# Optimization experiments

Hardware: AMD Instinct MI355X
Metric: run time of the kernel (lower is better)

## Reference

```python
import jax, jax.numpy as jnp
import numpy as np

B, L, CIN, COUT, HEADS = 8, 2048, 256, 256, 4
HD = COUT // HEADS
NEG_SLOPE = 0.2


def setup_inputs() -> dict:
    key = jax.random.key(0)
    k1, k2, k3, k4, k5 = jax.random.split(key, 5)
    x = jax.random.normal(k1, (B, L, CIN), dtype=jnp.float32)
    adj_mask = jax.random.randint(k2, (B, L, L), 0, 2) > 0  # bool [B,L,L]
    W = jax.random.normal(k3, (COUT, CIN), dtype=jnp.float32) * (1.0 / np.sqrt(CIN))
    att_src = jax.random.normal(k4, (1, HEADS, 1, HD), dtype=jnp.float32) * 0.1
    att_dst = jax.random.normal(k5, (1, HEADS, 1, HD), dtype=jnp.float32) * 0.1
    return {"x": x, "adj_mask": adj_mask, "W": W, "att_src": att_src, "att_dst": att_dst}


def reference(x, adj_mask, W, att_src, att_dst):
    Bb, Ll, _ = x.shape
    # linear projection (no bias), split heads: [B, H, L, D]
    h = jnp.einsum('blc,oc->blo', x, W).reshape(Bb, Ll, HEADS, HD).transpose(0, 2, 1, 3)
    # additive GAT scores
    a_src = jnp.sum(h * att_src, axis=-1, keepdims=True)          # [B,H,L,1]
    a_dst = jnp.sum(h * att_dst, axis=-1, keepdims=True)          # [B,H,L,1]
    e = a_src + jnp.swapaxes(a_dst, 2, 3)                          # [B,H,L,L]
    e = jnp.where(e >= 0, e, NEG_SLOPE * e)                        # leaky relu
    fill = jnp.finfo(e.dtype).min
    e = jnp.where(adj_mask[:, None, :, :], e, fill)                # mask non-edges
    alpha = jax.nn.softmax(e, axis=-1)                             # [B,H,L,L]
    # dropout is identity in eval/reference mode
    out = jnp.einsum('bhij,bhjd->bhid', alpha, h)                  # [B,H,L,D]
    return out.transpose(0, 2, 1, 3).reshape(Bb, Ll, COUT)
```

## Files before the change

### kernel.cpp

```cpp
#include <hip/hip_runtime.h>

#define B_ 8
#define L_ 2048
#define CIN_ 256
#define COUT_ 256
#define HEADS_ 4
#define HD_ 64
#define NEG_SLOPE_ 0.2f
#define LOG2E_ 1.4426950408889634f

#define TI 32
#define TJ 64
#define NJT (L_ / TJ)

typedef __attribute__((ext_vector_type(4))) float f32x4;
typedef __attribute__((ext_vector_type(8))) __bf16 bf16x8;
typedef __attribute__((ext_vector_type(4))) __bf16 bf16x4;


__global__ __launch_bounds__(256, 4)
void pack_kernel(const int* __restrict__ adj, unsigned long long* __restrict__ abitsT) {
  const size_t wid = ((size_t)blockIdx.x * 256 + threadIdx.x) >> 6;
  const int lane = threadIdx.x & 63;
  const int* p = adj + wid * 256 + lane;
  unsigned long long b0 = __ballot(p[0]   != 0);
  unsigned long long b1 = __ballot(p[64]  != 0);
  unsigned long long b2 = __ballot(p[128] != 0);
  unsigned long long b3 = __ballot(p[192] != 0);
  if (lane == 0) {
    const size_t row = wid >> 3;
    const int jw0 = (int)(wid & 7) * 4;
    const size_t bb = row >> 11, l = row & 2047;
    unsigned long long* dst = abitsT + (bb << 16) + l;
    dst[(size_t)(jw0 + 0) << 11] = b0;
    dst[(size_t)(jw0 + 1) << 11] = b1;
    dst[(size_t)(jw0 + 2) << 11] = b2;
    dst[(size_t)(jw0 + 3) << 11] = b3;
  }
}

__global__ __launch_bounds__(512, 2)
void proj_kernel(const float* __restrict__ x, const float* __restrict__ W,
                 const float* __restrict__ att_src, const float* __restrict__ att_dst,
                 __bf16* __restrict__ hF, float2* __restrict__ aE,
                 float2* __restrict__ aF) {
  __shared__ __align__(16) __bf16 Wl[COUT_][72];
  __shared__ __align__(16) __bf16 Al[2][2][512];

  const int tid = threadIdx.x;
  const int r0 = blockIdx.x * TI;
  const int b  = r0 >> 11;
  const int l0 = r0 & (L_ - 1);

  const int w8 = tid >> 6, lane = tid & 63, col = lane & 15, q = lane >> 4;
  const int h  = w8 & 3;
  const int mh = w8 >> 2;
  const int wrow = tid >> 3;
  const int wc8  = (tid & 7) * 8;
  const int si = tid >> 3, soct = tid & 7;

  f32x4 acc[4];
#pragma unroll
  for (int nt = 0; nt < 4; ++nt) acc[nt] = (f32x4)0.f;

  for (int kc = 0; kc < CIN_ / 64; ++kc) {
    __syncthreads();
#pragma unroll
    for (int rg = 0; rg < 4; ++rg) {
      const int row = rg * 64 + wrow;
      const float4* ws = (const float4*)(W + (size_t)row * CIN_ + kc * 64 + wc8);
#pragma unroll
      for (int u = 0; u < 2; ++u) {
        float4 f = ws[u];
        bf16x4 v;
        v[0] = (__bf16)f.x; v[1] = (__bf16)f.y; v[2] = (__bf16)f.z; v[3] = (__bf16)f.w;
        *(bf16x4*)&Wl[row][wc8 + u * 4] = v;
      }
    }
    if (tid < 256) {
      const float4* xs = (const float4*)(x + (size_t)(r0 + si) * CIN_ + kc * 64 + soct * 8);
      float4 f0 = xs[0], f1 = xs[1];
      bf16x8 v;
      v[0] = (__bf16)f0.x; v[1] = (__bf16)f0.y; v[2] = (__bf16)f0.z; v[3] = (__bf16)f0.w;
      v[4] = (__bf16)f1.x; v[5] = (__bf16)f1.y; v[6] = (__bf16)f1.z; v[7] = (__bf16)f1.w;
      *(bf16x8*)&Al[si >> 4][soct >> 2][(((soct & 3) << 4) + (si & 15)) << 3] = v;
    }
    __syncthreads();

    bf16x8 af[2], bfr[2][4];
#pragma unroll
    for (int kt = 0; kt < 2; ++kt)
      af[kt] = *(const bf16x8*)&Al[mh][kt][lane << 3];
#pragma unroll
    for (int kt = 0; kt < 2; ++kt)
#pragma unroll
      for (int nt = 0; nt < 4; ++nt)
        bfr[kt][nt] = *(const bf16x8*)&Wl[h * 64 + nt * 16 + col][kt * 32 + q * 8];
#pragma unroll
    for (int kt = 0; kt < 2; ++kt)
#pragma unroll
      for (int nt = 0; nt < 4; ++nt)
        acc[nt] = __builtin_amdgcn_mfma_f32_16x16x32_bf16(
            af[kt], bfr[kt][nt], acc[nt], 0, 0, 0);
  }

  float asv[4], adv[4];
#pragma unroll
  for (int nt = 0; nt < 4; ++nt) {
    asv[nt] = att_src[h * 64 + nt * 16 + col];
    adv[nt] = att_dst[h * 64 + nt * 16 + col];
  }
#pragma unroll
  for (int reg = 0; reg < 4; ++reg) {
    float s = 0.f, d = 0.f;
#pragma unroll
    for (int nt = 0; nt < 4; ++nt) {
      s = fmaf(acc[nt][reg], asv[nt], s);
      d = fmaf(acc[nt][reg], adv[nt], d);
    }
    s += __shfl_xor(s, 1, 64); d += __shfl_xor(d, 1, 64);
    s += __shfl_xor(s, 2, 64); d += __shfl_xor(d, 2, 64);
    s += __shfl_xor(s, 4, 64); d += __shfl_xor(d, 4, 64);
    s += __shfl_xor(s, 8, 64); d += __shfl_xor(d, 8, 64);
    if (col == 0) {
      const int il = mh * 16 + q * 4 + reg;
      const size_t idx = ((size_t)(b * HEADS_ + h) << 11) + l0 + il;
      float2 ev, fv;
      ev.x = __builtin_exp2f(s * LOG2E_);
      ev.y = __builtin_exp2f(s * (LOG2E_ * NEG_SLOPE_));
      fv.x = __builtin_exp2f(d * LOG2E_);
      fv.y = __builtin_exp2f(d * (LOG2E_ * NEG_SLOPE_));
      aE[idx] = ev;
      aF[idx] = fv;
    }
  }

  {
    const int jt_p = l0 >> 6;
    const int kt_p = (l0 >> 5) & 1;
    const int qhi = q >> 1, qlo = q & 1;
    const int qp = mh * 2 + qhi;
#pragma unroll
    for (int nt = 0; nt < 4; ++nt) {
      bf16x4 v;
      v[0] = (__bf16)acc[nt][0];
      v[1] = (__bf16)acc[nt][1];
      v[2] = (__bf16)acc[nt][2];
      v[3] = (__bf16)acc[nt][3];
      const size_t off =
          ((((size_t)(b * HEADS_ + h) * 32 + jt_p) * 2 + kt_p) * 4 + nt) * 512 +
          (qp * 16 + col) * 8 + qlo * 4;
      *(bf16x4*)(hF + off) = v;
    }
  }
}

__global__ __launch_bounds__(512, 2)
void attn_kernel(const __bf16* __restrict__ hF, const float2* __restrict__ aE,
                 const float2* __restrict__ aF,
                 const unsigned long long* __restrict__ abitsT,
                 float* __restrict__ out) {
  __shared__ __align__(16) float comb[HEADS_][64][36];

  const int tid = threadIdx.x;
  const int b  = blockIdx.x & 7;
  const int i0 = (blockIdx.x >> 3) * 32;

  const int w = tid >> 6, lane = tid & 63, col = lane & 15, q = lane >> 4;
  const int hh = w & 3;
  const int jh = w >> 2;
  const int jt0 = jh * (NJT / 2), jt1 = jt0 + NJT / 2;

  const size_t hl = (size_t)(b * HEADS_ + hh);
  const float2 EE[2] = {aE[(hl << 11) + i0 + col],
                        aE[(hl << 11) + i0 + 16 + col]};
  const float* afb = (const float*)(aF + (hl << 11)) + q * 16;
  const __bf16* hb = hF + hl * 131072 + lane * 8;
  const unsigned long long* mb = abitsT + ((size_t)b << 16) + i0 + col;

  f32x4 acc[2][4];
  float lsum[2] = {0.f, 0.f};
#pragma unroll
  for (int mt = 0; mt < 2; ++mt)
#pragma unroll
    for (int nt = 0; nt < 4; ++nt) acc[mt][nt] = (f32x4)0.f;

  for (int jt = jt0; jt < jt1; ++jt) {
    const unsigned long long cm0 = mb[(size_t)jt << 11];
    const unsigned long long cm1 = mb[((size_t)jt << 11) + 16];

#pragma unroll
    for (int kt = 0; kt < 2; ++kt) {
      bf16x8 cb0 = *(const bf16x8*)(hb + jt * 4096 + (kt * 4 + 0) * 512);
      bf16x8 cb1 = *(const bf16x8*)(hb + jt * 4096 + (kt * 4 + 1) * 512);
      bf16x8 cb2 = *(const bf16x8*)(hb + jt * 4096 + (kt * 4 + 2) * 512);
      bf16x8 cb3 = *(const bf16x8*)(hb + jt * 4096 + (kt * 4 + 3) * 512);
      float cf[16];
#pragma unroll
      for (int u = 0; u < 4; ++u)
        *(float4*)&cf[u * 4] =
            *(const float4*)(afb + jt * 128 + kt * 64 + u * 4);

      bf16x8 av[2];
#pragma unroll
      for (int mt = 0; mt < 2; ++mt) {
        const unsigned long long bw = mt ? cm1 : cm0;
        const unsigned int tsh = ((unsigned int)(bw >> (kt * 32))) >> (q * 8);
        const float Ex = EE[mt].x, Ey = EE[mt].y;
        float part = 0.f;
#pragma unroll
        for (int e = 0; e < 8; ++e) {
          const float m1 = Ex * cf[2 * e];
          const float m2 = Ey * cf[2 * e + 1];
          const float pm = fmaxf(m1, m2);
          const float p = (tsh & (1u << e)) ? pm : 0.f;
          part += p;
          av[mt][e] = (__bf16)p;
        }
        lsum[mt] += part;
      }
#pragma unroll
      for (int mt = 0; mt < 2; ++mt) {
        acc[mt][0] = __builtin_amdgcn_mfma_f32_16x16x32_bf16(av[mt], cb0, acc[mt][0], 0, 0, 0);
        acc[mt][1] = __builtin_amdgcn_mfma_f32_16x16x32_bf16(av[mt], cb1, acc[mt][1], 0, 0, 0);
        acc[mt][2] = __builtin_amdgcn_mfma_f32_16x16x32_bf16(av[mt], cb2, acc[mt][2], 0, 0, 0);
        acc[mt][3] = __builtin_amdgcn_mfma_f32_16x16x32_bf16(av[mt], cb3, acc[mt][3], 0, 0, 0);
      }
    }
  }

#pragma unroll
  for (int mt = 0; mt < 2; ++mt) {
    lsum[mt] += __shfl_xor(lsum[mt], 16, 64);
    lsum[mt] += __shfl_xor(lsum[mt], 32, 64);
  }

  if (jh == 1) {
#pragma unroll
    for (int mt = 0; mt < 2; ++mt)
#pragma unroll
      for (int nt = 0; nt < 4; ++nt)
        *(f32x4*)&comb[hh][lane][mt * 16 + nt * 4] = acc[mt][nt];
    comb[hh][lane][32] = lsum[0];
    comb[hh][lane][33] = lsum[1];
  }
  __syncthreads();
  if (jh == 0) {
#pragma unroll
    for (int mt = 0; mt < 2; ++mt) {
      const float ltot = lsum[mt] + comb[hh][lane][32 + mt];
#pragma unroll
      for (int reg = 0; reg < 4; ++reg) {
        const int m = q * 4 + reg;
        const float lm = __shfl(ltot, m, 64);
        const float linv = 1.0f / lm;
        const size_t orow =
            ((size_t)(b * L_ + i0 + mt * 16 + m)) * COUT_ + hh * 64;
#pragma unroll
        for (int nt = 0; nt < 4; ++nt) {
          const float v =
              acc[mt][nt][reg] + comb[hh][lane][mt * 16 + nt * 4 + reg];
          out[orow + nt * 16 + col] = v * linv;
        }
      }
    }
  }
}

extern "C" void kernel_launch(void* const* d_in, const int* in_sizes, int n_in,
                              void* d_out, int out_size, void* d_ws, size_t ws_size,
                              hipStream_t stream) {
  const float* x       = (const float*)d_in[0];
  const int*   adj     = (const int*)d_in[1];
  const float* W       = (const float*)d_in[2];
  const float* att_src = (const float*)d_in[3];
  const float* att_dst = (const float*)d_in[4];
  float* out = (float*)d_out;

  char* ws = (char*)d_ws;
  __bf16* hF = (__bf16*)ws;
  float2* aE = (float2*)(ws + (8u << 20));
  float2* aF = (float2*)(ws + (9u << 20));
  unsigned long long* abitsT =
      (unsigned long long*)(ws + (10u << 20));

  pack_kernel<<<(B_ * L_ * (L_ / 256)) / 4, 256, 0, stream>>>(adj, abitsT);
  proj_kernel<<<(B_ * L_) / TI, 512, 0, stream>>>(x, W, att_src, att_dst, hF, aE, aF);
  attn_kernel<<<B_ * (L_ / 32), 512, 0, stream>>>(hF, aE, aF, abitsT, out);
}
```

Before: 263.3 us.

## Share per-head value tiles through double-buffered LDS across eight row-waves

The attention kernel is reorganized so each block handles one batch/head and 256 query rows, with each of its eight waves owning 32 rows and sweeping all key tiles. Value tiles are staged cooperatively into a double-buffered LDS buffer and reused by all waves, replacing per-wave global loads. The cross-wave split over keys and its LDS combine step are removed. In exchange, each block waits on a barrier every key tile, and the grid shrinks to 256 blocks, which lowers parallelism.

```diff
diff --git a/kernel.cpp b/kernel.cpp
--- a/kernel.cpp
+++ b/kernel.cpp
@@ -155,28 +155,27 @@
   }
 }
 
-__global__ __launch_bounds__(512, 2)
+__global__ __launch_bounds__(512)
 void attn_kernel(const __bf16* __restrict__ hF, const float2* __restrict__ aE,
                  const float2* __restrict__ aF,
                  const unsigned long long* __restrict__ abitsT,
                  float* __restrict__ out) {
-  __shared__ __align__(16) float comb[HEADS_][64][36];
+  __shared__ __align__(16) __bf16 kv[2][4096];
 
   const int tid = threadIdx.x;
   const int b  = blockIdx.x & 7;
-  const int i0 = (blockIdx.x >> 3) * 32;
+  const int hh = (blockIdx.x >> 3) & 3;
+  const int ib = blockIdx.x >> 5;
 
   const int w = tid >> 6, lane = tid & 63, col = lane & 15, q = lane >> 4;
-  const int hh = w & 3;
-  const int jh = w >> 2;
-  const int jt0 = jh * (NJT / 2), jt1 = jt0 + NJT / 2;
+  const int iw0 = ib * 256 + w * 32;
 
   const size_t hl = (size_t)(b * HEADS_ + hh);
-  const float2 EE[2] = {aE[(hl << 11) + i0 + col],
-                        aE[(hl << 11) + i0 + 16 + col]};
+  const float2 EE[2] = {aE[(hl << 11) + iw0 + col],
+                        aE[(hl << 11) + iw0 + 16 + col]};
   const float* afb = (const float*)(aF + (hl << 11)) + q * 16;
-  const __bf16* hb = hF + hl * 131072 + lane * 8;
-  const unsigned long long* mb = abitsT + ((size_t)b << 16) + i0 + col;
+  const __bf16* hbase = hF + hl * 131072;
+  const unsigned long long* mb = abitsT + ((size_t)b << 16) + iw0 + col;
 
   f32x4 acc[2][4];
   float lsum[2] = {0.f, 0.f};
@@ -185,16 +184,27 @@
 #pragma unroll
     for (int nt = 0; nt < 4; ++nt) acc[mt][nt] = (f32x4)0.f;
 
-  for (int jt = jt0; jt < jt1; ++jt) {
+  {
+    float4 r0 = *(const float4*)(hbase + tid * 8);
+    *(float4*)((char*)&kv[0][0] + tid * 16) = r0;
+  }
+  __syncthreads();
+
+  int cur = 0;
+  for (int jt = 0; jt < NJT; ++jt) {
+    float4 rnext;
+    if (jt < NJT - 1)
+      rnext = *(const float4*)(hbase + (size_t)(jt + 1) * 4096 + tid * 8);
+
     const unsigned long long cm0 = mb[(size_t)jt << 11];
     const unsigned long long cm1 = mb[((size_t)jt << 11) + 16];
 
 #pragma unroll
     for (int kt = 0; kt < 2; ++kt) {
-      bf16x8 cb0 = *(const bf16x8*)(hb + jt * 4096 + (kt * 4 + 0) * 512);
-      bf16x8 cb1 = *(const bf16x8*)(hb + jt * 4096 + (kt * 4 + 1) * 512);
-      bf16x8 cb2 = *(const bf16x8*)(hb + jt * 4096 + (kt * 4 + 2) * 512);
-      bf16x8 cb3 = *(const bf16x8*)(hb + jt * 4096 + (kt * 4 + 3) * 512);
+      bf16x8 cb0 = *(const bf16x8*)&kv[cur][(kt * 4 + 0) * 512 + lane * 8];
+      bf16x8 cb1 = *(const bf16x8*)&kv[cur][(kt * 4 + 1) * 512 + lane * 8];
+      bf16x8 cb2 = *(const bf16x8*)&kv[cur][(kt * 4 + 2) * 512 + lane * 8];
+      bf16x8 cb3 = *(const bf16x8*)&kv[cur][(kt * 4 + 3) * 512 + lane * 8];
       float cf[16];
 #pragma unroll
       for (int u = 0; u < 4; ++u)
@@ -227,6 +237,11 @@
         acc[mt][3] = __builtin_amdgcn_mfma_f32_16x16x32_bf16(av[mt], cb3, acc[mt][3], 0, 0, 0);
       }
     }
+
+    if (jt < NJT - 1)
+      *(float4*)((char*)&kv[cur ^ 1][0] + tid * 16) = rnext;
+    __syncthreads();
+    cur ^= 1;
   }
 
 #pragma unroll
@@ -235,34 +250,18 @@
     lsum[mt] += __shfl_xor(lsum[mt], 32, 64);
   }
 
-  if (jh == 1) {
-#pragma unroll
-    for (int mt = 0; mt < 2; ++mt)
+#pragma unroll
+  for (int mt = 0; mt < 2; ++mt) {
+#pragma unroll
+    for (int reg = 0; reg < 4; ++reg) {
+      const int m = q * 4 + reg;
+      const float lm = __shfl(lsum[mt], m, 64);
+      const float linv = 1.0f / lm;
+      const size_t orow =
+          ((size_t)(b * L_ + iw0 + mt * 16 + m)) * COUT_ + hh * 64;
 #pragma unroll
       for (int nt = 0; nt < 4; ++nt)
-        *(f32x4*)&comb[hh][lane][mt * 16 + nt * 4] = acc[mt][nt];
-    comb[hh][lane][32] = lsum[0];
-    comb[hh][lane][33] = lsum[1];
-  }
-  __syncthreads();
-  if (jh == 0) {
-#pragma unroll
-    for (int mt = 0; mt < 2; ++mt) {
-      const float ltot = lsum[mt] + comb[hh][lane][32 + mt];
-#pragma unroll
-      for (int reg = 0; reg < 4; ++reg) {
-        const int m = q * 4 + reg;
-        const float lm = __shfl(ltot, m, 64);
-        const float linv = 1.0f / lm;
-        const size_t orow =
-            ((size_t)(b * L_ + i0 + mt * 16 + m)) * COUT_ + hh * 64;
-#pragma unroll
-        for (int nt = 0; nt < 4; ++nt) {
-          const float v =
-              acc[mt][nt][reg] + comb[hh][lane][mt * 16 + nt * 4 + reg];
-          out[orow + nt * 16 + col] = v * linv;
-        }
-      }
+        out[orow + nt * 16 + col] = acc[mt][nt][reg] * linv;
     }
   }
 }
@@ -286,5 +285,5 @@
 
   pack_kernel<<<(B_ * L_ * (L_ / 256)) / 4, 256, 0, stream>>>(adj, abitsT);
   proj_kernel<<<(B_ * L_) / TI, 512, 0, stream>>>(x, W, att_src, att_dst, hF, aE, aF);
-  attn_kernel<<<B_ * (L_ / 32), 512, 0, stream>>>(hF, aE, aF, abitsT, out);
-}
+  attn_kernel<<<B_ * HEADS_ * (L_ / 256), 512, 0, stream>>>(hF, aE, aF, abitsT, out);
+}
```

Result: slower. 271.9 us (+3.3%).

## Fuse adjacency bit-packing into projection kernel and compute row sums via MFMA

Applied to the files above, without the earlier changes.

Removes the separate pack kernel and folds adjacency bit-packing into the projection kernel: each wave loads a mask row into registers before the GEMM step and ballots it afterward, so the adjacency read overlaps the projection compute. In the attention kernel, the per-row softmax denominators are now accumulated with an extra MFMA against a vector of ones instead of scalar adds and cross-lane shuffles. The mask words for the next tile are prefetched one iteration ahead, and the min-waves hint is dropped from launch bounds. The cost is higher register pressure in proj (32 preloaded ints per thread) and one extra MFMA per tile, while the row sums are now taken from bf16-rounded probabilities.

```diff
diff --git a/kernel.cpp b/kernel.cpp
--- a/kernel.cpp
+++ b/kernel.cpp
@@ -18,30 +18,10 @@
 typedef __attribute__((ext_vector_type(4))) __bf16 bf16x4;
 
 
-__global__ __launch_bounds__(256, 4)
-void pack_kernel(const int* __restrict__ adj, unsigned long long* __restrict__ abitsT) {
-  const size_t wid = ((size_t)blockIdx.x * 256 + threadIdx.x) >> 6;
-  const int lane = threadIdx.x & 63;
-  const int* p = adj + wid * 256 + lane;
-  unsigned long long b0 = __ballot(p[0]   != 0);
-  unsigned long long b1 = __ballot(p[64]  != 0);
-  unsigned long long b2 = __ballot(p[128] != 0);
-  unsigned long long b3 = __ballot(p[192] != 0);
-  if (lane == 0) {
-    const size_t row = wid >> 3;
-    const int jw0 = (int)(wid & 7) * 4;
-    const size_t bb = row >> 11, l = row & 2047;
-    unsigned long long* dst = abitsT + (bb << 16) + l;
-    dst[(size_t)(jw0 + 0) << 11] = b0;
-    dst[(size_t)(jw0 + 1) << 11] = b1;
-    dst[(size_t)(jw0 + 2) << 11] = b2;
-    dst[(size_t)(jw0 + 3) << 11] = b3;
-  }
-}
-
 __global__ __launch_bounds__(512, 2)
 void proj_kernel(const float* __restrict__ x, const float* __restrict__ W,
                  const float* __restrict__ att_src, const float* __restrict__ att_dst,
+                 const int* __restrict__ adj, unsigned long long* __restrict__ abitsT,
                  __bf16* __restrict__ hF, float2* __restrict__ aE,
                  float2* __restrict__ aF) {
   __shared__ __align__(16) __bf16 Wl[COUT_][72];
@@ -64,6 +44,12 @@
   for (int nt = 0; nt < 4; ++nt) acc[nt] = (f32x4)0.f;
 
   for (int kc = 0; kc < CIN_ / 64; ++kc) {
+    const int prow = l0 + w8 * 4 + kc;
+    const int* ap = adj + (((size_t)(b * L_ + prow)) << 11) + lane;
+    int pv[32];
+#pragma unroll
+    for (int c = 0; c < 32; ++c) pv[c] = ap[c * 64];
+
     __syncthreads();
 #pragma unroll
     for (int rg = 0; rg < 4; ++rg) {
@@ -102,6 +88,13 @@
       for (int nt = 0; nt < 4; ++nt)
         acc[nt] = __builtin_amdgcn_mfma_f32_16x16x32_bf16(
             af[kt], bfr[kt][nt], acc[nt], 0, 0, 0);
+
+#pragma unroll
+    for (int c = 0; c < 32; ++c) {
+      const unsigned long long m = __ballot(pv[c] != 0);
+      if (lane == 0)
+        abitsT[((size_t)b << 16) + ((size_t)c << 11) + prow] = m;
+    }
   }
 
   float asv[4], adv[4];
@@ -155,12 +148,12 @@
   }
 }
 
-__global__ __launch_bounds__(512, 2)
+__global__ __launch_bounds__(512)
 void attn_kernel(const __bf16* __restrict__ hF, const float2* __restrict__ aE,
                  const float2* __restrict__ aF,
                  const unsigned long long* __restrict__ abitsT,
                  float* __restrict__ out) {
-  __shared__ __align__(16) float comb[HEADS_][64][36];
+  __shared__ __align__(16) float comb[HEADS_][64][40];
 
   const int tid = threadIdx.x;
   const int b  = blockIdx.x & 7;
@@ -178,16 +171,25 @@
   const __bf16* hb = hF + hl * 131072 + lane * 8;
   const unsigned long long* mb = abitsT + ((size_t)b << 16) + i0 + col;
 
-  f32x4 acc[2][4];
-  float lsum[2] = {0.f, 0.f};
-#pragma unroll
-  for (int mt = 0; mt < 2; ++mt)
+  bf16x8 bones;
+#pragma unroll
+  for (int e = 0; e < 8; ++e) bones[e] = (__bf16)1.0f;
+
+  f32x4 acc[2][4], accl[2];
+#pragma unroll
+  for (int mt = 0; mt < 2; ++mt) {
+    accl[mt] = (f32x4)0.f;
 #pragma unroll
     for (int nt = 0; nt < 4; ++nt) acc[mt][nt] = (f32x4)0.f;
+  }
+
+  unsigned long long cm0 = mb[(size_t)jt0 << 11];
+  unsigned long long cm1 = mb[((size_t)jt0 << 11) + 16];
 
   for (int jt = jt0; jt < jt1; ++jt) {
-    const unsigned long long cm0 = mb[(size_t)jt << 11];
-    const unsigned long long cm1 = mb[((size_t)jt << 11) + 16];
+    const int jn = (jt < jt1 - 1) ? jt + 1 : jt;
+    const unsigned long long nm0 = mb[(size_t)jn << 11];
+    const unsigned long long nm1 = mb[((size_t)jn << 11) + 16];
 
 #pragma unroll
     for (int kt = 0; kt < 2; ++kt) {
@@ -207,17 +209,14 @@
         const unsigned long long bw = mt ? cm1 : cm0;
         const unsigned int tsh = ((unsigned int)(bw >> (kt * 32))) >> (q * 8);
         const float Ex = EE[mt].x, Ey = EE[mt].y;
-        float part = 0.f;
 #pragma unroll
         for (int e = 0; e < 8; ++e) {
           const float m1 = Ex * cf[2 * e];
           const float m2 = Ey * cf[2 * e + 1];
           const float pm = fmaxf(m1, m2);
           const float p = (tsh & (1u << e)) ? pm : 0.f;
-          part += p;
           av[mt][e] = (__bf16)p;
         }
-        lsum[mt] += part;
       }
 #pragma unroll
       for (int mt = 0; mt < 2; ++mt) {
@@ -225,14 +224,11 @@
         acc[mt][1] = __builtin_amdgcn_mfma_f32_16x16x32_bf16(av[mt], cb1, acc[mt][1], 0, 0, 0);
         acc[mt][2] = __builtin_amdgcn_mfma_f32_16x16x32_bf16(av[mt], cb2, acc[mt][2], 0, 0, 0);
         acc[mt][3] = __builtin_amdgcn_mfma_f32_16x16x32_bf16(av[mt], cb3, acc[mt][3], 0, 0, 0);
-      }
-    }
-  }
-
-#pragma unroll
-  for (int mt = 0; mt < 2; ++mt) {
-    lsum[mt] += __shfl_xor(lsum[mt], 16, 64);
-    lsum[mt] += __shfl_xor(lsum[mt], 32, 64);
+        accl[mt] = __builtin_amdgcn_mfma_f32_16x16x32_bf16(av[mt], bones, accl[mt], 0, 0, 0);
+      }
+    }
+
+    cm0 = nm0; cm1 = nm1;
   }
 
   if (jh == 1) {
@@ -241,19 +237,18 @@
 #pragma unroll
       for (int nt = 0; nt < 4; ++nt)
         *(f32x4*)&comb[hh][lane][mt * 16 + nt * 4] = acc[mt][nt];
-    comb[hh][lane][32] = lsum[0];
-    comb[hh][lane][33] = lsum[1];
+    *(f32x4*)&comb[hh][lane][32] = accl[0];
+    *(f32x4*)&comb[hh][lane][36] = accl[1];
   }
   __syncthreads();
   if (jh == 0) {
 #pragma unroll
     for (int mt = 0; mt < 2; ++mt) {
-      const float ltot = lsum[mt] + comb[hh][lane][32 + mt];
+      const f32x4 lo = accl[mt] + *(const f32x4*)&comb[hh][lane][32 + mt * 4];
 #pragma unroll
       for (int reg = 0; reg < 4; ++reg) {
         const int m = q * 4 + reg;
-        const float lm = __shfl(ltot, m, 64);
-        const float linv = 1.0f / lm;
+        const float linv = 1.0f / lo[reg];
         const size_t orow =
             ((size_t)(b * L_ + i0 + mt * 16 + m)) * COUT_ + hh * 64;
 #pragma unroll
@@ -284,7 +279,7 @@
   unsigned long long* abitsT =
       (unsigned long long*)(ws + (10u << 20));
 
-  pack_kernel<<<(B_ * L_ * (L_ / 256)) / 4, 256, 0, stream>>>(adj, abitsT);
-  proj_kernel<<<(B_ * L_) / TI, 512, 0, stream>>>(x, W, att_src, att_dst, hF, aE, aF);
+  proj_kernel<<<(B_ * L_) / TI, 512, 0, stream>>>(
+      x, W, att_src, att_dst, adj, abitsT, hF, aE, aF);
   attn_kernel<<<B_ * (L_ / 32), 512, 0, stream>>>(hF, aE, aF, abitsT, out);
 }
```

New measurement: 262.0 us. Within noise of the previous version (-0.5%).
